# Optimization experiments

Measured on AMD Instinct MI355X. Metric: run time of the kernel, lower is better.

## Reference

```python
import jax, jax.numpy as jnp
import numpy as np

ATT_DIM = 2048
NUM_HEADS = 16
NUM_KV_GROUPS = 4
HEAD_DIM = 128
CONTEXT_LENGTH = 2048
ROPE_BASE = 10000.0
GROUP_SIZE = NUM_HEADS // NUM_KV_GROUPS
BATCH = 2


def _precompute_rope_sin(context_length, head_dim, rope_base):
    # thetas over rope_dim = head_dim // 2, exponent uses rope_dim (as in source)
    rope_dim = head_dim // 2
    j = jnp.arange(rope_dim, dtype=jnp.float32)
    thetas = 1.0 / rope_base ** (2.0 * j / rope_dim)
    positions = jnp.arange(context_length, dtype=jnp.float32)
    angles = positions[:, None] * thetas[None, :]          # [CD, HD//2]
    angles = jnp.concatenate([angles, angles], axis=-1)    # [CD, HD]
    return jnp.sin(angles)                                  # cos is unused (see bug note)


def _apply_rope(qk, sin):
    # FAITHFUL to source bug: in compute_rope, `cos` is overwritten with the
    # broadcast `sin`, so the returned value is qk*sin + qk_2*sin.
    hd = qk.shape[-1]
    qkr = qk[..., : hd // 2]
    qki = qk[..., hd // 2 :]
    qk2 = jnp.concatenate([-qki, qkr], axis=-1)
    sin_b = sin[None, None, : qk.shape[2], :]
    return qk * sin_b + qk2 * sin  # second term broadcasts full-length sin (requires cd==context_length)


def setup_inputs() -> dict:
    key = jax.random.key(0)
    ks = jax.random.split(key, 6)
    s = 0.02
    x = jax.random.normal(ks[0], (BATCH, CONTEXT_LENGTH, ATT_DIM), dtype=jnp.float32)
    Wq = jax.random.normal(ks[1], (ATT_DIM, HEAD_DIM * NUM_HEADS), dtype=jnp.float32) * s
    Wk = jax.random.normal(ks[2], (ATT_DIM, HEAD_DIM * NUM_KV_GROUPS), dtype=jnp.float32) * s
    Wv = jax.random.normal(ks[3], (ATT_DIM, HEAD_DIM * NUM_KV_GROUPS), dtype=jnp.float32) * s
    Wo = jax.random.normal(ks[4], (HEAD_DIM * NUM_HEADS, HEAD_DIM * NUM_HEADS), dtype=jnp.float32) * s
    bo = jax.random.normal(ks[5], (HEAD_DIM * NUM_HEADS,), dtype=jnp.float32) * s
    return {"x": x, "Wq": Wq, "Wk": Wk, "Wv": Wv, "Wo": Wo, "bo": bo}


def reference(x, Wq, Wk, Wv, Wo, bo):
    bd, cd, ed = x.shape
    sin = _precompute_rope_sin(CONTEXT_LENGTH, HEAD_DIM, ROPE_BASE)

    q = (x @ Wq).reshape(bd, cd, NUM_HEADS, HEAD_DIM).transpose(0, 2, 1, 3)      # [B,NH,CD,HD]
    k = (x @ Wk).reshape(bd, cd, NUM_KV_GROUPS, HEAD_DIM).transpose(0, 2, 1, 3)  # [B,Nkv,CD,HD]
    v = (x @ Wv).reshape(bd, cd, NUM_KV_GROUPS, HEAD_DIM).transpose(0, 2, 1, 3)

    q = _apply_rope(q, sin)
    k = _apply_rope(k, sin)

    k = jnp.repeat(k, GROUP_SIZE, axis=1)  # [B,NH,CD,HD]
    v = jnp.repeat(v, GROUP_SIZE, axis=1)

    a = jnp.einsum("bhqd,bhkd->bhqk", q, k)  # [B,NH,CD,CD]
    causal = jnp.triu(jnp.ones((cd, cd), dtype=bool), k=1)
    a = jnp.where(causal[None, None], -jnp.inf, a)
    a = jax.nn.softmax(a / jnp.sqrt(jnp.float32(HEAD_DIM)), axis=-1)

    y = jnp.einsum("bhqk,bhkd->bhqd", a, v)                # [B,NH,CD,HD]
    y = y.transpose(0, 2, 1, 3).reshape(bd, cd, HEAD_DIM * NUM_HEADS)
    return y @ Wo + bo
```

## Files before the change

kernel.cpp:

```cpp
#include <hip/hip_runtime.h>
#include <hip/hip_bf16.h>
#include <cstdint>
#include <cstddef>

#define BATCH 2
#define CTX 2048
#define EMB 2048
#define NH 16
#define NG 4
#define HD 128
#define NQK (EMB + 2*NG*HD)
#define MROWS (BATCH*CTX)

typedef __bf16 bf16x8 __attribute__((ext_vector_type(8)));
typedef float  f32x4  __attribute__((ext_vector_type(4)));
typedef float  f32x16 __attribute__((ext_vector_type(16)));

__device__ __forceinline__ ushort f2bf(float f) {
    uint32_t u = __float_as_uint(f);
    u += 0x7FFFu + ((u >> 16) & 1u);
    return (ushort)(u >> 16);
}

__device__ __forceinline__ float bf2f(ushort u) {
    return __uint_as_float((uint32_t)u << 16);
}

__device__ __forceinline__ uint32_t packbf(float a, float b) {
    ushort lo = __builtin_bit_cast(ushort, (__bf16)a);
    ushort hi = __builtin_bit_cast(ushort, (__bf16)b);
    return (uint32_t)lo | ((uint32_t)hi << 16);
}

__device__ __forceinline__ bf16x8 mkfrag(uint32_t a, uint32_t b, uint32_t c, uint32_t d) {
    union { uint32_t u[4]; bf16x8 v; } z;
    z.u[0] = a; z.u[1] = b; z.u[2] = c; z.u[3] = d;
    return z.v;
}

__device__ __forceinline__ void gload_lds16(const void* g, void* l) {
    __builtin_amdgcn_global_load_lds((const __attribute__((address_space(1))) void*)g,
                                     (__attribute__((address_space(3))) void*)l, 16, 0, 0);
}

__global__ __launch_bounds__(256) void k_sintab(float* __restrict__ sintab) {
    int t = blockIdx.x * 256 + threadIdx.x;
    int j = t & 63, p = t >> 6;
    float theta = 1.0f / powf(10000.0f, (float)(2 * j) / 64.0f);
    sintab[t] = sinf((float)p * theta);
}

__global__ __launch_bounds__(256) void k_cvt(const float4* __restrict__ src, ushort4* __restrict__ dst) {
    int i = blockIdx.x * 256 + threadIdx.x;
    float4 v = src[i];
    ushort4 o;
    o.x = f2bf(v.x); o.y = f2bf(v.y); o.z = f2bf(v.z); o.w = f2bf(v.w);
    dst[i] = o;
}

__global__ __launch_bounds__(256) void k_transpose_all(const float* __restrict__ Wq, const float* __restrict__ Wk,
                                                       const float* __restrict__ Wv, const float* __restrict__ Wo,
                                                       ushort* __restrict__ Wt, ushort* __restrict__ Wot) {
    __shared__ float tile[32][33];
    int z = blockIdx.z;
    const float* src; ushort* dst; int src_ld, dst_ld, ncols;
    if (z == 0)      { src = Wq; dst = Wt;                              src_ld = EMB;   dst_ld = EMB; ncols = EMB; }
    else if (z == 1) { src = Wk; dst = Wt + (size_t)EMB * EMB;          src_ld = NG*HD; dst_ld = EMB; ncols = NG*HD; }
    else if (z == 2) { src = Wv; dst = Wt + (size_t)(EMB + NG*HD) * EMB; src_ld = NG*HD; dst_ld = EMB; ncols = NG*HD; }
    else             { src = Wo; dst = Wot;                             src_ld = EMB;   dst_ld = EMB; ncols = EMB; }
    int c0 = blockIdx.x * 32, r0 = blockIdx.y * 32;
    if (c0 >= ncols) return;
    int tx = threadIdx.x, ty = threadIdx.y;
    #pragma unroll
    for (int i = 0; i < 4; ++i)
        tile[ty + i*8][tx] = src[(size_t)(r0 + ty + i*8) * src_ld + c0 + tx];
    __syncthreads();
    #pragma unroll
    for (int i = 0; i < 4; ++i)
        dst[(size_t)(c0 + ty + i*8) * dst_ld + r0 + tx] = f2bf(tile[tx][ty + i*8]);
}

#define CLDS_STRIDE 130
__global__ __launch_bounds__(256) void k_gemm_qkv(const ushort* __restrict__ A, const ushort* __restrict__ Bt,
                                                  const float* __restrict__ sintab,
                                                  ushort* __restrict__ Qf, ushort* __restrict__ Kf,
                                                  ushort* __restrict__ Vf, float qscale) {
    __shared__ __align__(16) char smem[33792];
    int tid = threadIdx.x;
    int lane = tid & 63;
    int wave = tid >> 6;
    int wr = wave >> 1, wc = wave & 1;

    int nbx = gridDim.x;
    int id  = blockIdx.y * nbx + blockIdx.x;
    int cpx = (nbx * gridDim.y) >> 3;
    int sid = (id & 7) * cpx + (id >> 3);
    int bx = sid % nbx, by = sid / nbx;
    int m0 = by * 128, n0 = bx * 128;

    int lr = lane & 15, lg = lane >> 4;

    f32x4 acc[4][4] = {};

    int arow = lane >> 2;
    int kpart = (lane & 3) * 8;

    ushort* As = (ushort*)smem;
    ushort* Bs = (ushort*)(smem + 16384);

    int c0s = (wave*2 + 0) * 512, c1s = (wave*2 + 1) * 512;
    const ushort* ga0 = A  + (size_t)(m0 + (wave*2+0)*16 + arow) * EMB + kpart;
    const ushort* ga1 = A  + (size_t)(m0 + (wave*2+1)*16 + arow) * EMB + kpart;
    const ushort* gb0 = Bt + (size_t)(n0 + (wave*2+0)*16 + arow) * EMB + kpart;
    const ushort* gb1 = Bt + (size_t)(n0 + (wave*2+1)*16 + arow) * EMB + kpart;

    auto stage = [&](int koff, int bufoff) {
        gload_lds16(ga0 + koff, &As[bufoff + c0s]);
        gload_lds16(ga1 + koff, &As[bufoff + c1s]);
        gload_lds16(gb0 + koff, &Bs[bufoff + c0s]);
        gload_lds16(gb1 + koff, &Bs[bufoff + c1s]);
    };
    auto compute = [&](int bufoff) {
        bf16x8 af[4], bfr[4];
        #pragma unroll
        for (int mt = 0; mt < 4; ++mt)
            af[mt] = *(const bf16x8*)&As[bufoff + (wr*64 + mt*16 + lr) * 32 + lg * 8];
        #pragma unroll
        for (int nt = 0; nt < 4; ++nt)
            bfr[nt] = *(const bf16x8*)&Bs[bufoff + (wc*64 + nt*16 + lr) * 32 + lg * 8];
        #pragma unroll
        for (int mt = 0; mt < 4; ++mt)
            #pragma unroll
            for (int nt = 0; nt < 4; ++nt)
                acc[mt][nt] = __builtin_amdgcn_mfma_f32_16x16x32_bf16(af[mt], bfr[nt], acc[mt][nt], 0, 0, 0);
    };

    const int nsteps = EMB / 32;
    stage(0, 0);
    __syncthreads();
    for (int t = 0; t + 2 < nsteps; t += 2) {
        stage(32, 4096);
        compute(0);
        __syncthreads();
        stage(64, 0);
        compute(4096);
        __syncthreads();
        ga0 += 64; ga1 += 64; gb0 += 64; gb1 += 64;
    }
    stage(32, 4096);
    compute(0);
    __syncthreads();
    compute(4096);
    __syncthreads();

    ushort* clds = (ushort*)smem;
    #pragma unroll
    for (int mt = 0; mt < 4; ++mt) {
        #pragma unroll
        for (int nt = 0; nt < 4; ++nt) {
            int col = wc*64 + nt*16 + lr;
            int row = wr*64 + mt*16 + lg*4;
            ushort2 p01, p23;
            p01.x = f2bf(acc[mt][nt][0]); p01.y = f2bf(acc[mt][nt][1]);
            p23.x = f2bf(acc[mt][nt][2]); p23.y = f2bf(acc[mt][nt][3]);
            *(ushort2*)&clds[col*CLDS_STRIDE + row]     = p01;
            *(ushort2*)&clds[col*CLDS_STRIDE + row + 2] = p23;
        }
    }
    __syncthreads();

    int xt = bx;
    int b = m0 >> 11;
    int pos0 = m0 & 2047;

    if (xt < 20) {
        int j = tid & 63;
        int rgrp = tid >> 6;
        ushort* dstb;
        float scl;
        if (xt < 16) { dstb = Qf + (size_t)((b*NH + xt) * 64) * 4096;      scl = qscale; }
        else         { dstb = Kf + (size_t)((b*NG + (xt-16)) * 64) * 4096; scl = 1.0f;   }
        #pragma unroll 4
        for (int it = 0; it < 32; ++it) {
            int row = rgrp + it*4;
            int pos = pos0 + row;
            float a  = bf2f(clds[j*CLDS_STRIDE + row]);
            float bb = bf2f(clds[(j+64)*CLDS_STRIDE + row]);
            float sv = sintab[pos*64 + j] * scl;
            size_t idx = (size_t)(pos>>5)*4096 + (size_t)(j>>4)*512 + ((j>>3)&1)*256 + (pos&31)*8 + (j&7);
            dstb[idx]        = f2bf((a - bb) * sv);
            dstb[idx + 2048] = f2bf((bb + a) * sv);
        }
    } else {
        int g = xt - 20;
        int bg = b*NG + g;
        int ln2 = tid & 31, hi2 = (tid >> 5) & 1, dt = tid >> 6;
        int colc = dt*32 + ln2;
        #pragma unroll
        for (int stp = 0; stp < 4; ++stp) {
            #pragma unroll
            for (int ks = 0; ks < 2; ++ks) {
                int rowb = stp*32 + ks*16 + hi2*8;
                union { ushort2 q[4]; bf16x8 v; } z;
                z.q[0] = *(ushort2*)&clds[colc*CLDS_STRIDE + rowb];
                z.q[1] = *(ushort2*)&clds[colc*CLDS_STRIDE + rowb + 2];
                z.q[2] = *(ushort2*)&clds[colc*CLDS_STRIDE + rowb + 4];
                z.q[3] = *(ushort2*)&clds[colc*CLDS_STRIDE + rowb + 6];
                int step_g = (pos0 >> 5) + stp;
                *(bf16x8*)(Vf + ((size_t)(bg*64 + step_g)*8 + dt*2 + ks) * 512 + (tid & 63) * 8) = z.v;
            }
        }
    }
}

__global__ __launch_bounds__(256) void k_gemm_bt(const ushort* __restrict__ A, const ushort* __restrict__ Bt,
                                                 float* __restrict__ C, int M, int N, int K,
                                                 const float* __restrict__ bias) {
    __shared__ __align__(16) ushort As[2][128 * 32];
    __shared__ __align__(16) ushort Bs[2][128 * 32];
    int tid = threadIdx.x;
    int lane = tid & 63;
    int wave = tid >> 6;
    int wr = wave >> 1, wc = wave & 1;

    int nbx = gridDim.x;
    int id  = blockIdx.y * nbx + blockIdx.x;
    int cpx = (nbx * gridDim.y) >> 3;
    int sid = (id & 7) * cpx + (id >> 3);
    int bx = sid % nbx, by = sid / nbx;
    int m0 = by * 128, n0 = bx * 128;

    int lr = lane & 15, lg = lane >> 4;

    f32x4 acc[4][4] = {};

    int arow = lane >> 2;
    int kpart = (lane & 3) * 8;

    int c0s = (wave*2 + 0) * 512, c1s = (wave*2 + 1) * 512;
    const ushort* ga0 = A  + (size_t)(m0 + (wave*2+0)*16 + arow) * K + kpart;
    const ushort* ga1 = A  + (size_t)(m0 + (wave*2+1)*16 + arow) * K + kpart;
    const ushort* gb0 = Bt + (size_t)(n0 + (wave*2+0)*16 + arow) * K + kpart;
    const ushort* gb1 = Bt + (size_t)(n0 + (wave*2+1)*16 + arow) * K + kpart;

    auto stage = [&](int koff, int buf) {
        gload_lds16(ga0 + koff, &As[buf][c0s]);
        gload_lds16(ga1 + koff, &As[buf][c1s]);
        gload_lds16(gb0 + koff, &Bs[buf][c0s]);
        gload_lds16(gb1 + koff, &Bs[buf][c1s]);
    };
    auto compute = [&](int buf) {
        bf16x8 af[4], bfr[4];
        #pragma unroll
        for (int mt = 0; mt < 4; ++mt)
            af[mt] = *(const bf16x8*)&As[buf][(wr*64 + mt*16 + lr) * 32 + lg * 8];
        #pragma unroll
        for (int nt = 0; nt < 4; ++nt)
            bfr[nt] = *(const bf16x8*)&Bs[buf][(wc*64 + nt*16 + lr) * 32 + lg * 8];
        #pragma unroll
        for (int mt = 0; mt < 4; ++mt)
            #pragma unroll
            for (int nt = 0; nt < 4; ++nt)
                acc[mt][nt] = __builtin_amdgcn_mfma_f32_16x16x32_bf16(af[mt], bfr[nt], acc[mt][nt], 0, 0, 0);
    };

    int nsteps = K >> 5;
    stage(0, 0);
    __syncthreads();
    for (int t = 0; t + 2 < nsteps; t += 2) {
        stage(32, 1);
        compute(0);
        __syncthreads();
        stage(64, 0);
        compute(1);
        __syncthreads();
        ga0 += 64; ga1 += 64; gb0 += 64; gb1 += 64;
    }
    stage(32, 1);
    compute(0);
    __syncthreads();
    compute(1);

    #pragma unroll
    for (int mt = 0; mt < 4; ++mt) {
        #pragma unroll
        for (int nt = 0; nt < 4; ++nt) {
            int col = n0 + wc*64 + nt*16 + lr;
            float bv = bias ? bias[col] : 0.0f;
            #pragma unroll
            for (int r = 0; r < 4; ++r) {
                int row = m0 + wr*64 + mt*16 + lg*4 + r;
                C[(size_t)row * N + col] = acc[mt][nt][r] + bv;
            }
        }
    }
}

__global__ __launch_bounds__(128) void k_attn13(const ushort* __restrict__ Qf, const ushort* __restrict__ Kf,
                                                const ushort* __restrict__ Vf, ushort* __restrict__ y) {
    __shared__ __align__(16) char smem[16640];
    char*  Qs  = smem;
    float* sOd = (float*)smem;
    float* sl  = (float*)(smem + 16384);

    int lane = threadIdx.x & 63;
    int w    = threadIdx.x >> 6;
    int B  = blockIdx.x;
    int bg = B & 7;
    int within = B >> 3;
    int t  = 63 - (within >> 2);
    int hh = within & 3;
    int b = bg >> 2, g = bg & 3, h = g * 4 + hh;
    int ln = lane & 31, hi = lane >> 5;
    int q0 = t * 32;

    {
        const ushort* qf_g = Qf + ((size_t)((b*NH + h) * 64 + t)) * 4096;
        int tid = threadIdx.x;
        #pragma unroll
        for (int it = 0; it < 4; ++it)
            gload_lds16(qf_g + (it*128 + tid) * 8, Qs + it*2048 + w*1024);
    }
    __syncthreads();

    const ushort* kfb = Kf + (size_t)bg * 64 * 4096 + lane * 8;
    const ushort* vfb = Vf + (size_t)bg * 64 * 4096 + lane * 8;
    const char*   qsl = Qs + lane * 16;

    f32x16 od[4] = {};
    float lsum = 0.0f;

    auto step = [&](int si, bool diag) {
        const ushort* kp = kfb + (size_t)si * 4096;
        const ushort* vp = vfb + (size_t)si * 4096;
        f32x16 st = {};
        #pragma unroll
        for (int s = 0; s < 8; ++s) {
            bf16x8 kf = *(const bf16x8*)(kp + s * 512);
            bf16x8 qf = *(const bf16x8*)(qsl + s * 1024);
            st = __builtin_amdgcn_mfma_f32_32x32x16_bf16(kf, qf, st, 0, 0, 0);
        }

        if (diag) {
            #pragma unroll
            for (int r = 0; r < 16; ++r) {
                int kl = (r & 3) + 8*(r >> 2) + 4*hi;
                if (kl > ln) st[r] = -1e30f;
            }
        }
        #pragma unroll
        for (int r = 0; r < 16; ++r) st[r] = exp2f(st[r]);
        float s8[8];
        #pragma unroll
        for (int r = 0; r < 8; ++r) s8[r] = st[r] + st[r+8];
        #pragma unroll
        for (int r = 0; r < 4; ++r) s8[r] = s8[r] + s8[r+4];
        lsum += (s8[0] + s8[1]) + (s8[2] + s8[3]);

        #pragma unroll
        for (int ks = 0; ks < 2; ++ks) {
            uint32_t w0 = packbf(st[8*ks+0], st[8*ks+1]);
            uint32_t w1 = packbf(st[8*ks+2], st[8*ks+3]);
            uint32_t w2 = packbf(st[8*ks+4], st[8*ks+5]);
            uint32_t w3 = packbf(st[8*ks+6], st[8*ks+7]);
            uint32_t sa = hi ? w0 : w2;
            uint32_t sb = hi ? w1 : w3;
            uint32_t ra = (uint32_t)__shfl_xor((int)sa, 32, 64);
            uint32_t rb = (uint32_t)__shfl_xor((int)sb, 32, 64);
            bf16x8 pa = hi ? mkfrag(ra, rb, w2, w3) : mkfrag(w0, w1, ra, rb);
            #pragma unroll
            for (int dt = 0; dt < 4; ++dt) {
                bf16x8 vf = *(const bf16x8*)(vp + (dt*2 + ks) * 512);
                od[dt] = __builtin_amdgcn_mfma_f32_32x32x16_bf16(pa, vf, od[dt], 0, 0, 0);
            }
        }
    };

    for (int si = w; si < t; si += 2) step(si, false);
    if ((t & 1) == w) step(t, true);

    lsum += __shfl_xor(lsum, 32, 64);

    __syncthreads();
    if (w == 1) {
        #pragma unroll
        for (int r = 0; r < 16; ++r) {
            int ri = (r & 3) + 8*(r >> 2) + 4*hi;
            #pragma unroll
            for (int dt = 0; dt < 4; ++dt) sOd[ri*128 + dt*32 + ln] = od[dt][r];
        }
        if (hi == 0) sl[ln] = lsum;
    }
    __syncthreads();
    if (w == 0) {
        float inv = 1.0f / (lsum + sl[ln]);
        #pragma unroll
        for (int r = 0; r < 16; ++r) {
            int ri = (r & 3) + 8*(r >> 2) + 4*hi;
            float ivr = __shfl(inv, ri, 64);
            int row = q0 + ri;
            #pragma unroll
            for (int dt = 0; dt < 4; ++dt) {
                float v = (od[dt][r] + sOd[ri*128 + dt*32 + ln]) * ivr;
                y[((size_t)(b*CTX + row)) * (NH*HD) + h*HD + dt*32 + ln] = f2bf(v);
            }
        }
    }
}

#define SIN_OFF   ((size_t)0)
#define XB_OFF    ((size_t)524288)
#define WT_OFF    ((size_t)17301504)
#define WOT_OFF   ((size_t)29884416)
#define QB_OFF    ((size_t)88604672)
#define KB_OFF    ((size_t)105381888)
#define VT_OFF    ((size_t)109576192)
#define YB_OFF    ((size_t)113770496)

extern "C" void kernel_launch(void* const* d_in, const int* in_sizes, int n_in,
                              void* d_out, int out_size, void* d_ws, size_t ws_size,
                              hipStream_t stream) {
    const float* x  = (const float*)d_in[0];
    const float* Wq = (const float*)d_in[1];
    const float* Wk = (const float*)d_in[2];
    const float* Wv = (const float*)d_in[3];
    const float* Wo = (const float*)d_in[4];
    const float* bo = (const float*)d_in[5];
    float* out = (float*)d_out;
    char* ws = (char*)d_ws;

    float*  sintab = (float*)(ws + SIN_OFF);
    ushort* xb     = (ushort*)(ws + XB_OFF);
    ushort* Wt     = (ushort*)(ws + WT_OFF);
    ushort* Wot    = (ushort*)(ws + WOT_OFF);
    ushort* Qf     = (ushort*)(ws + QB_OFF);
    ushort* Kf     = (ushort*)(ws + KB_OFF);
    ushort* Vf     = (ushort*)(ws + VT_OFF);
    ushort* yb     = (ushort*)(ws + YB_OFF);

    const float qscale = 0.08838834764831845f * 1.4426950408889634f;

    k_sintab<<<512, 256, 0, stream>>>(sintab);
    k_cvt<<<(MROWS * EMB / 4) / 256, 256, 0, stream>>>((const float4*)x, (ushort4*)xb);
    k_transpose_all<<<dim3(64, 64, 4), dim3(32, 8), 0, stream>>>(Wq, Wk, Wv, Wo, Wt, Wot);
    k_gemm_qkv<<<dim3(NQK/128, MROWS/128), 256, 0, stream>>>(xb, Wt, sintab, Qf, Kf, Vf, qscale);
    k_attn13<<<2048, 128, 0, stream>>>(Qf, Kf, Vf, yb);
    k_gemm_bt<<<dim3(EMB/128, MROWS/128), 256, 0, stream>>>(yb, Wot, out, MROWS, EMB, EMB, bo);
}
```

Baseline: 207.0 us.

## Share K/V tiles across GQA heads via LDS in 512-thread attention blocks

Reorganizes the attention kernel so that one 512-thread block handles all four query heads of a KV group for a query tile. K and V tiles are staged cooperatively into shared memory and reused by all heads, instead of each head reading them straight from global memory. This cuts redundant global/L2 traffic for K/V by about the group size. The cost is a __syncthreads per round with no double buffering, larger LDS use (about 66KB) and fewer, bigger blocks, which may reduce occupancy and overlap.

```diff
diff --git a/kernel.cpp b/kernel.cpp
--- a/kernel.cpp
+++ b/kernel.cpp
@@ -296,51 +296,55 @@
     }
 }
 
-__global__ __launch_bounds__(128) void k_attn13(const ushort* __restrict__ Qf, const ushort* __restrict__ Kf,
+__global__ __launch_bounds__(512) void k_attn14(const ushort* __restrict__ Qf, const ushort* __restrict__ Kf,
                                                 const ushort* __restrict__ Vf, ushort* __restrict__ y) {
-    __shared__ __align__(16) char smem[16640];
-    char*  Qs  = smem;
-    float* sOd = (float*)smem;
-    float* sl  = (float*)(smem + 16384);
-
-    int lane = threadIdx.x & 63;
-    int w    = threadIdx.x >> 6;
+    __shared__ __align__(16) char smem[66048];
+
+    int tid  = threadIdx.x;
+    int lane = tid & 63;
+    int w    = tid >> 6;
+    int hh   = w >> 1, ww = w & 1;
     int B  = blockIdx.x;
     int bg = B & 7;
-    int within = B >> 3;
-    int t  = 63 - (within >> 2);
-    int hh = within & 3;
+    int t  = 63 - (B >> 3);
     int b = bg >> 2, g = bg & 3, h = g * 4 + hh;
     int ln = lane & 31, hi = lane >> 5;
     int q0 = t * 32;
 
-    {
-        const ushort* qf_g = Qf + ((size_t)((b*NH + h) * 64 + t)) * 4096;
-        int tid = threadIdx.x;
-        #pragma unroll
-        for (int it = 0; it < 4; ++it)
-            gload_lds16(qf_g + (it*128 + tid) * 8, Qs + it*2048 + w*1024);
-    }
-    __syncthreads();
-
-    const ushort* kfb = Kf + (size_t)bg * 64 * 4096 + lane * 8;
-    const ushort* vfb = Vf + (size_t)bg * 64 * 4096 + lane * 8;
-    const char*   qsl = Qs + lane * 16;
+    const ushort* kf_g = Kf + (size_t)bg * 64 * 4096;
+    const ushort* vf_g = Vf + (size_t)bg * 64 * 4096;
+
+    auto stageKV = [&](int r) {
+        #pragma unroll
+        for (int s2 = 0; s2 < 2; ++s2) {
+            gload_lds16(kf_g + r*8192 + s2*4096 + tid*8, smem + 32768 + s2*8192 + tid*16);
+            gload_lds16(vf_g + r*8192 + s2*4096 + tid*8, smem + 49152 + s2*8192 + tid*16);
+        }
+    };
+
+    #pragma unroll
+    for (int s = 0; s < 4; ++s) {
+        const ushort* qsrc = Qf + ((size_t)((b*NH + g*4 + s) * 64 + t)) * 4096 + tid * 8;
+        gload_lds16(qsrc, smem + s*8192 + tid*16);
+    }
+    stageKV(0);
+    __syncthreads();
+
+    const char* qsl = smem + hh*8192  + lane*16;
+    const char* ksl = smem + 32768 + ww*8192 + lane*16;
+    const char* vsl = smem + 49152 + ww*8192 + lane*16;
 
     f32x16 od[4] = {};
     float lsum = 0.0f;
 
-    auto step = [&](int si, bool diag) {
-        const ushort* kp = kfb + (size_t)si * 4096;
-        const ushort* vp = vfb + (size_t)si * 4096;
+    auto step = [&](bool diag) {
         f32x16 st = {};
         #pragma unroll
         for (int s = 0; s < 8; ++s) {
-            bf16x8 kf = *(const bf16x8*)(kp + s * 512);
+            bf16x8 kf = *(const bf16x8*)(ksl + s * 1024);
             bf16x8 qf = *(const bf16x8*)(qsl + s * 1024);
             st = __builtin_amdgcn_mfma_f32_32x32x16_bf16(kf, qf, st, 0, 0, 0);
         }
-
         if (diag) {
             #pragma unroll
             for (int r = 0; r < 16; ++r) {
@@ -370,19 +374,28 @@
             bf16x8 pa = hi ? mkfrag(ra, rb, w2, w3) : mkfrag(w0, w1, ra, rb);
             #pragma unroll
             for (int dt = 0; dt < 4; ++dt) {
-                bf16x8 vf = *(const bf16x8*)(vp + (dt*2 + ks) * 512);
+                bf16x8 vf = *(const bf16x8*)(vsl + (dt*2 + ks) * 1024);
                 od[dt] = __builtin_amdgcn_mfma_f32_32x32x16_bf16(pa, vf, od[dt], 0, 0, 0);
             }
         }
     };
 
-    for (int si = w; si < t; si += 2) step(si, false);
-    if ((t & 1) == w) step(t, true);
+    int rounds = (t >> 1) + 1;
+    for (int r = 0; r < rounds; ++r) {
+        int tile = 2*r + ww;
+        if (tile <= t) step(tile == t);
+        __syncthreads();
+        if (r + 1 < rounds) {
+            stageKV(r + 1);
+            __syncthreads();
+        }
+    }
 
     lsum += __shfl_xor(lsum, 32, 64);
 
-    __syncthreads();
-    if (w == 1) {
+    float* sOd = (float*)(smem + hh*16512);
+    float* sl  = (float*)(smem + hh*16512 + 16384);
+    if (ww == 1) {
         #pragma unroll
         for (int r = 0; r < 16; ++r) {
             int ri = (r & 3) + 8*(r >> 2) + 4*hi;
@@ -392,7 +405,7 @@
         if (hi == 0) sl[ln] = lsum;
     }
     __syncthreads();
-    if (w == 0) {
+    if (ww == 0) {
         float inv = 1.0f / (lsum + sl[ln]);
         #pragma unroll
         for (int r = 0; r < 16; ++r) {
@@ -444,6 +457,6 @@
     k_cvt<<<(MROWS * EMB / 4) / 256, 256, 0, stream>>>((const float4*)x, (ushort4*)xb);
     k_transpose_all<<<dim3(64, 64, 4), dim3(32, 8), 0, stream>>>(Wq, Wk, Wv, Wo, Wt, Wot);
     k_gemm_qkv<<<dim3(NQK/128, MROWS/128), 256, 0, stream>>>(xb, Wt, sintab, Qf, Kf, Vf, qscale);
-    k_attn13<<<2048, 128, 0, stream>>>(Qf, Kf, Vf, yb);
+    k_attn14<<<512, 512, 0, stream>>>(Qf, Kf, Vf, yb);
     k_gemm_bt<<<dim3(EMB/128, MROWS/128), 256, 0, stream>>>(yb, Wot, out, MROWS, EMB, EMB, bo);
 }
```

Result: no change. 207.7 us (+0.3%).
